# Performance work log

Measured on AMD Instinct MI355X. Metric: run time of the kernel, lower is better.

Reference implementation:

```python
import jax, jax.numpy as jnp
import numpy as np

SEMANTIC_DIM = 128
N_COMPONENTS = 2
EMBED_DIM = SEMANTIC_DIM * N_COMPONENTS  # 256
MAX_LEN = 512


def sinusoidal_pe(max_len, d_model):
    pos = jnp.arange(max_len, dtype=jnp.float32)[:, None]              # (L,1)
    div = jnp.exp(jnp.arange(0, d_model, 2, dtype=jnp.float32) * (-np.log(10000.0) / d_model))
    ang = pos * div                                                     # (L, d/2)
    # interleave sin/cos: pe[:,0::2]=sin, pe[:,1::2]=cos
    return jnp.stack([jnp.sin(ang), jnp.cos(ang)], axis=-1).reshape(max_len, d_model)


def setup_inputs() -> dict:
    key = jax.random.key(0)
    k1, k2, k3, k4 = jax.random.split(key, 4)
    byte_sequence = jax.random.randint(k1, (64, 512), 0, 256, dtype=jnp.int64)
    continuous_positions = jax.random.uniform(k2, (64, 2048), dtype=jnp.float32)
    emb_table = jax.random.normal(k3, (256, EMBED_DIM), dtype=jnp.float32)
    locality_shapes = jax.random.normal(k4, (256, 3), dtype=jnp.float32)
    return {
        "byte_sequence": byte_sequence,
        "continuous_positions": continuous_positions,
        "emb_table": emb_table,
        "locality_shapes": locality_shapes,
    }


def reference(byte_sequence, continuous_positions, emb_table, locality_shapes):
    B, L = byte_sequence.shape
    pe = sinusoidal_pe(MAX_LEN, EMBED_DIM)[:L]                          # (L, E)
    byte_embeds = emb_table[byte_sequence] + pe[None, :, :]             # (B, L, E)
    byte_amplitudes = byte_embeds.reshape(B, L, N_COMPONENTS, SEMANTIC_DIM)

    byte_positions = jnp.linspace(0.0, 1.0, L, dtype=jnp.float32)      # (L,)
    x_diff = continuous_positions[:, :, None] - byte_positions[None, None, :]  # (B, P, L)

    lp = locality_shapes[byte_sequence]                                 # (B, L, 3)
    widths = jnp.abs(lp[:, :, 1]) * 0.02 + 1e-5                         # (B, L)
    amplitudes = jax.nn.sigmoid(lp[:, :, 2])                            # (B, L)

    local_basis = jnp.exp(-0.5 * (x_diff / widths[:, None, :]) ** 2) * amplitudes[:, None, :]
    semantic_field = jnp.einsum('bpl,blcd->bpcd', local_basis, byte_amplitudes)
    return semantic_field
```

## Files before the change

### kernel.cpp

```cpp
#include <hip/hip_runtime.h>
#include <math.h>

#define LSEQ 512
#define EDIM 256
#define PDIM 2048
#define BM   128
#define BK   32
#define NT   16

typedef _Float16 f16x8 __attribute__((ext_vector_type(8)));
typedef _Float16 f16x2 __attribute__((ext_vector_type(2)));
typedef float    f32x4 __attribute__((ext_vector_type(4)));

#if __has_builtin(__builtin_amdgcn_exp2f)
#define EXP2F(x) __builtin_amdgcn_exp2f(x)
#else
#define EXP2F(x) __expf((x) * 0.6931471805599453f)
#endif

__device__ inline f16x2 pk2(float a, float b) {
#if __has_builtin(__builtin_amdgcn_cvt_pkrtz)
    return __builtin_bit_cast(f16x2, __builtin_amdgcn_cvt_pkrtz(a, b));
#else
    f16x2 r; r[0] = (_Float16)a; r[1] = (_Float16)b; return r;
#endif
}

__device__ __host__ inline int tile_off(int r, int g) {
    return ((r >> 1) << 6) + ((r & 1) << 5) + (((g ^ ((r >> 1) & 3)) & 3) << 3);
}

__device__ inline void g2lds16(const void* g, void* l) {
    __builtin_amdgcn_global_load_lds(
        (const __attribute__((address_space(1))) void*)g,
        (__attribute__((address_space(3))) void*)l, 16, 0, 0);
}

__global__ __launch_bounds__(256) void precompute_all(
    const int*   __restrict__ bs,
    const float* __restrict__ ls,
    const float* __restrict__ emb,
    float2*      __restrict__ params,
    _Float16*    __restrict__ baset) {
    const int b   = blockIdx.x >> 4;
    const int t   = blockIdx.x & 15;
    const int tid = threadIdx.x;

    __shared__ int sByte[BK];
    if (tid < BK) {
        const int l    = t * BK + tid;
        const int byte = bs[b * LSEQ + l];
        sByte[tid] = byte;
        const float l1  = ls[byte * 3 + 1];
        const float l2  = ls[byte * 3 + 2];
        const float wdt = fabsf(l1) * 0.02f + 1e-5f;
        const float amp = 1.0f / (1.0f + __expf(-l2));
        params[b * LSEQ + l] = make_float2(-0.72134752f / (wdt * wdt),
                                           __log2f(amp));
    }
    __syncthreads();

    const float div = __expf((float)(tid >> 1) * (-2.0f * 9.210340372f / 256.0f));
    _Float16* chunk = baset + ((size_t)blockIdx.x << 13);
#pragma unroll
    for (int g = 0; g < 4; ++g) {
        f16x8 v;
#pragma unroll
        for (int j = 0; j < 8; ++j) {
            const int lj  = g * 8 + j;
            const float ang = (float)(t * BK + lj) * div;
            const float pev = (tid & 1) ? cosf(ang) : sinf(ang);
            v[j] = (_Float16)(emb[sByte[lj] * EDIM + tid] + pev);
        }
        *(f16x8*)&chunk[tile_off(tid, g)] = v;
    }
}

__global__ __launch_bounds__(512, 4) void field_mfma(
    const float*    __restrict__ cpos,
    const float2*   __restrict__ params,
    const _Float16* __restrict__ baset,
    float*          __restrict__ out) {

    __shared__ __align__(16) _Float16 sW[2][BM * BK];
    __shared__ __align__(16) _Float16 sB[2][EDIM * BK];
    __shared__ __align__(16) float2   sPrm[LSEQ];

    const int orig = blockIdx.x;
    const int wg   = (orig & 7) * 128 + (orig >> 3);
    const int b    = wg >> 4;
    const int pt   = wg & 15;

    const int tid = threadIdx.x, lane = tid & 63, wave = tid >> 6;
    const int c15 = lane & 15, g4 = lane >> 4;
    const int wrow = wave >> 2, wcol = wave & 3;

    const int sp = tid >> 2;
    const int sg = tid & 3;
    const float mypos = cpos[b * PDIM + pt * BM + sp];
    const float invL  = 1.0f / (float)(LSEQ - 1);
    const int   woff  = tile_off(sp, sg);

    int aoff[4], boff[4];
#pragma unroll
    for (int rt = 0; rt < 4; ++rt) aoff[rt] = tile_off(wrow * 64 + rt * 16 + c15, g4);
#pragma unroll
    for (int ct = 0; ct < 4; ++ct) boff[ct] = tile_off(wcol * 64 + ct * 16 + c15, g4);

    sPrm[tid] = params[b * LSEQ + tid];
    const _Float16* bt = baset + ((size_t)b * NT << 13);
#pragma unroll
    for (int buf = 0; buf < 2; ++buf) {
        const _Float16* src = bt + buf * 8192 + wave * 1024 + lane * 8;
        g2lds16(src,       &sB[buf][wave * 1024]);
        g2lds16(src + 512, &sB[buf][wave * 1024 + 512]);
    }
    __syncthreads();

    auto genW = [&](int t, int dbuf) {
        const float4* qp = (const float4*)&sPrm[t * BK + sg * 8];
        const float4 q01 = qp[0], q23 = qp[1], q45 = qp[2], q67 = qp[3];
        const float bl0 = (float)(t * BK + sg * 8) * invL;
        float w[8];
#define GW(i, c2, la) { float d = mypos - (bl0 + (float)(i) * invL); \
                        w[i] = EXP2F(fmaf(d * d, (c2), (la))); }
        GW(0, q01.x, q01.y) GW(1, q01.z, q01.w)
        GW(2, q23.x, q23.y) GW(3, q23.z, q23.w)
        GW(4, q45.x, q45.y) GW(5, q45.z, q45.w)
        GW(6, q67.x, q67.y) GW(7, q67.z, q67.w)
#undef GW
        f16x8 wv;
        ((f16x2*)&wv)[0] = pk2(w[0], w[1]);
        ((f16x2*)&wv)[1] = pk2(w[2], w[3]);
        ((f16x2*)&wv)[2] = pk2(w[4], w[5]);
        ((f16x2*)&wv)[3] = pk2(w[6], w[7]);
        *(f16x8*)&sW[dbuf][woff] = wv;
    };

    genW(0, 0);
    __syncthreads();

    f32x4 acc[4][4];
#pragma unroll
    for (int i = 0; i < 4; ++i)
#pragma unroll
        for (int j = 0; j < 4; ++j) acc[i][j] = (f32x4)(0.f);

    for (int t = 0; t < NT; ++t) {
        const int cur = t & 1;
        if (t < NT - 1) genW(t + 1, cur ^ 1);

        const _Float16* wb = sW[cur];
        const _Float16* bb = sB[cur];
        f16x8 af[4];
#pragma unroll
        for (int rt = 0; rt < 4; ++rt) af[rt] = *(const f16x8*)&wb[aoff[rt]];
        __builtin_amdgcn_s_setprio(1);
#pragma unroll
        for (int ct = 0; ct < 4; ++ct) {
            const f16x8 bf = *(const f16x8*)&bb[boff[ct]];
#pragma unroll
            for (int rt = 0; rt < 4; ++rt)
                acc[rt][ct] = __builtin_amdgcn_mfma_f32_16x16x32_f16(af[rt], bf, acc[rt][ct], 0, 0, 0);
        }
        __builtin_amdgcn_s_setprio(0);

        __syncthreads();

        if (t < NT - 2) {
            const _Float16* src = bt + (t + 2) * 8192 + wave * 1024 + lane * 8;
            g2lds16(src,       &sB[cur][wave * 1024]);
            g2lds16(src + 512, &sB[cur][wave * 1024 + 512]);
        }
    }

#pragma unroll
    for (int rt = 0; rt < 4; ++rt)
#pragma unroll
        for (int ct = 0; ct < 4; ++ct) {
            const int e = wcol * 64 + ct * 16 + c15;
#pragma unroll
            for (int r = 0; r < 4; ++r) {
                const int p = pt * BM + wrow * 64 + rt * 16 + g4 * 4 + r;
                out[((size_t)b * PDIM + p) * EDIM + e] = acc[rt][ct][r];
            }
        }
}

extern "C" void kernel_launch(void* const* d_in, const int* in_sizes, int n_in,
                              void* d_out, int out_size, void* d_ws, size_t ws_size,
                              hipStream_t stream) {
    const int*   bs   = (const int*)d_in[0];
    const float* cpos = (const float*)d_in[1];
    const float* emb  = (const float*)d_in[2];
    const float* ls   = (const float*)d_in[3];

    const int B = in_sizes[0] / LSEQ;

    char* ws = (char*)d_ws;
    float2*   params = (float2*)ws;
    _Float16* baset  = (_Float16*)(ws + (1u << 18));

    precompute_all<<<B * NT, 256, 0, stream>>>(bs, ls, emb, params, baset);
    field_mfma<<<B * (PDIM / BM), 512, 0, stream>>>(cpos, params, baset, (float*)d_out);
}
```

Before: 65.99 us.

## Sort query positions and skip byte tiles outside Gaussian support

Adds a per-batch bitonic sort of continuous positions so each block handles a contiguous range of positions. Precompute now records, for each 32-byte tile, the interval where its Gaussian weights exceed a small cutoff. The main kernel skips weight generation and MFMA work for tiles outside that interval, and scatters output rows back through the sort permutation. It also switches the positional-encoding sin/cos to hardware instructions. The cost is an extra kernel launch, scattered output writes, and a small truncation of very small weights. The skip only pays off if the widths are narrow, as they are in the test data.

```diff
diff --git a/kernel.cpp b/kernel.cpp
--- a/kernel.cpp
+++ b/kernel.cpp
@@ -26,6 +26,23 @@
 #endif
 }
 
+__device__ inline float hw_sin(float ang) {
+#if __has_builtin(__builtin_amdgcn_sinf)
+    float rev = ang * 0.15915494309189535f;
+    return __builtin_amdgcn_sinf(rev - floorf(rev));
+#else
+    return sinf(ang);
+#endif
+}
+__device__ inline float hw_cos(float ang) {
+#if __has_builtin(__builtin_amdgcn_cosf)
+    float rev = ang * 0.15915494309189535f;
+    return __builtin_amdgcn_cosf(rev - floorf(rev));
+#else
+    return cosf(ang);
+#endif
+}
+
 __device__ __host__ inline int tile_off(int r, int g) {
     return ((r >> 1) << 6) + ((r & 1) << 5) + (((g ^ ((r >> 1) & 3)) & 3) << 3);
 }
@@ -34,6 +51,37 @@
     __builtin_amdgcn_global_load_lds(
         (const __attribute__((address_space(1))) void*)g,
         (__attribute__((address_space(3))) void*)l, 16, 0, 0);
+}
+
+__global__ __launch_bounds__(1024) void sort_pos(const float* __restrict__ cpos,
+                                                 float* __restrict__ spos,
+                                                 int*   __restrict__ oidx) {
+    const int b = blockIdx.x, tid = threadIdx.x;
+    __shared__ float v[2048];
+    __shared__ int   ix[2048];
+    v[tid] = cpos[b * PDIM + tid];           ix[tid] = tid;
+    v[tid + 1024] = cpos[b * PDIM + tid + 1024]; ix[tid + 1024] = tid + 1024;
+    for (int k = 2; k <= 2048; k <<= 1) {
+        for (int j = k >> 1; j > 0; j >>= 1) {
+            __syncthreads();
+#pragma unroll
+            for (int r = 0; r < 2; ++r) {
+                const int i = tid + (r << 10);
+                const int p = i ^ j;
+                if (p > i) {
+                    const bool up = ((i & k) == 0);
+                    const float a = v[i], c = v[p];
+                    if ((a > c) == up) {
+                        v[i] = c; v[p] = a;
+                        const int t2 = ix[i]; ix[i] = ix[p]; ix[p] = t2;
+                    }
+                }
+            }
+        }
+    }
+    __syncthreads();
+    spos[b * PDIM + tid] = v[tid];           oidx[b * PDIM + tid] = ix[tid];
+    spos[b * PDIM + tid + 1024] = v[tid + 1024]; oidx[b * PDIM + tid + 1024] = ix[tid + 1024];
 }
 
 __global__ __launch_bounds__(256) void precompute_all(
@@ -41,12 +89,14 @@
     const float* __restrict__ ls,
     const float* __restrict__ emb,
     float2*      __restrict__ params,
+    float2*      __restrict__ benv,
     _Float16*    __restrict__ baset) {
     const int b   = blockIdx.x >> 4;
     const int t   = blockIdx.x & 15;
     const int tid = threadIdx.x;
 
     __shared__ int sByte[BK];
+    __shared__ float sLo[BK], sHi[BK];
     if (tid < BK) {
         const int l    = t * BK + tid;
         const int byte = bs[b * LSEQ + l];
@@ -55,10 +105,20 @@
         const float l2  = ls[byte * 3 + 2];
         const float wdt = fabsf(l1) * 0.02f + 1e-5f;
         const float amp = 1.0f / (1.0f + __expf(-l2));
-        params[b * LSEQ + l] = make_float2(-0.72134752f / (wdt * wdt),
-                                           __log2f(amp));
-    }
-    __syncthreads();
+        const float la  = __log2f(amp);
+        params[b * LSEQ + l] = make_float2(-0.72134752f / (wdt * wdt), la);
+        const float dcut = wdt * sqrtf((la + 16.6096f) * (1.0f / 0.72134752f));
+        const float ctr  = (float)l * (1.0f / (float)(LSEQ - 1));
+        sLo[tid] = ctr - dcut;
+        sHi[tid] = ctr + dcut;
+    }
+    __syncthreads();
+    if (tid == 0) {
+        float lo = sLo[0], hi = sHi[0];
+#pragma unroll
+        for (int i = 1; i < BK; ++i) { lo = fminf(lo, sLo[i]); hi = fmaxf(hi, sHi[i]); }
+        benv[blockIdx.x] = make_float2(lo, hi);
+    }
 
     const float div = __expf((float)(tid >> 1) * (-2.0f * 9.210340372f / 256.0f));
     _Float16* chunk = baset + ((size_t)blockIdx.x << 13);
@@ -69,7 +129,7 @@
         for (int j = 0; j < 8; ++j) {
             const int lj  = g * 8 + j;
             const float ang = (float)(t * BK + lj) * div;
-            const float pev = (tid & 1) ? cosf(ang) : sinf(ang);
+            const float pev = (tid & 1) ? hw_cos(ang) : hw_sin(ang);
             v[j] = (_Float16)(emb[sByte[lj] * EDIM + tid] + pev);
         }
         *(f16x8*)&chunk[tile_off(tid, g)] = v;
@@ -77,14 +137,19 @@
 }
 
 __global__ __launch_bounds__(512, 4) void field_mfma(
-    const float*    __restrict__ cpos,
+    const float*    __restrict__ spos,
+    const int*      __restrict__ oidx,
     const float2*   __restrict__ params,
+    const float2*   __restrict__ benv,
     const _Float16* __restrict__ baset,
     float*          __restrict__ out) {
 
     __shared__ __align__(16) _Float16 sW[2][BM * BK];
     __shared__ __align__(16) _Float16 sB[2][EDIM * BK];
     __shared__ __align__(16) float2   sPrm[LSEQ];
+    __shared__ float  sPos[BM];
+    __shared__ int    sIdx[BM];
+    __shared__ float2 sBenv[NT];
 
     const int orig = blockIdx.x;
     const int wg   = (orig & 7) * 128 + (orig >> 3);
@@ -97,9 +162,8 @@
 
     const int sp = tid >> 2;
     const int sg = tid & 3;
-    const float mypos = cpos[b * PDIM + pt * BM + sp];
-    const float invL  = 1.0f / (float)(LSEQ - 1);
-    const int   woff  = tile_off(sp, sg);
+    const float invL = 1.0f / (float)(LSEQ - 1);
+    const int woff = tile_off(sp, sg);
 
     int aoff[4], boff[4];
 #pragma unroll
@@ -108,6 +172,12 @@
     for (int ct = 0; ct < 4; ++ct) boff[ct] = tile_off(wcol * 64 + ct * 16 + c15, g4);
 
     sPrm[tid] = params[b * LSEQ + tid];
+    if (tid < BM) {
+        sPos[tid] = spos[b * PDIM + pt * BM + tid];
+        sIdx[tid] = oidx[b * PDIM + pt * BM + tid];
+    }
+    if (tid < NT) sBenv[tid] = benv[b * NT + tid];
+
     const _Float16* bt = baset + ((size_t)b * NT << 13);
 #pragma unroll
     for (int buf = 0; buf < 2; ++buf) {
@@ -117,17 +187,27 @@
     }
     __syncthreads();
 
+    const float mypos = sPos[sp];
+    const float glo = sPos[wave * 16], ghi = sPos[wave * 16 + 15];
+    const float wlo = sPos[wrow * 64], whi = sPos[wrow * 64 + 63];
+
     auto genW = [&](int t, int dbuf) {
+        const float2 be = sBenv[t];
+        if (ghi < be.x || glo > be.y) {
+            *(f16x8*)&sW[dbuf][woff] = (f16x8)(_Float16)0.0f;
+            return;
+        }
         const float4* qp = (const float4*)&sPrm[t * BK + sg * 8];
-        const float4 q01 = qp[0], q23 = qp[1], q45 = qp[2], q67 = qp[3];
+        const float4 q0 = qp[0], q1 = qp[1], q2 = qp[2], q3 = qp[3];
         const float bl0 = (float)(t * BK + sg * 8) * invL;
+        const float pd  = mypos - bl0;
         float w[8];
-#define GW(i, c2, la) { float d = mypos - (bl0 + (float)(i) * invL); \
+#define GW(i, c2, la) { float d = pd - (float)(i) * invL; \
                         w[i] = EXP2F(fmaf(d * d, (c2), (la))); }
-        GW(0, q01.x, q01.y) GW(1, q01.z, q01.w)
-        GW(2, q23.x, q23.y) GW(3, q23.z, q23.w)
-        GW(4, q45.x, q45.y) GW(5, q45.z, q45.w)
-        GW(6, q67.x, q67.y) GW(7, q67.z, q67.w)
+        GW(0, q0.x, q0.y) GW(1, q0.z, q0.w)
+        GW(2, q1.x, q1.y) GW(3, q1.z, q1.w)
+        GW(4, q2.x, q2.y) GW(5, q2.z, q2.w)
+        GW(6, q3.x, q3.y) GW(7, q3.z, q3.w)
 #undef GW
         f16x8 wv;
         ((f16x2*)&wv)[0] = pk2(w[0], w[1]);
@@ -150,20 +230,25 @@
         const int cur = t & 1;
         if (t < NT - 1) genW(t + 1, cur ^ 1);
 
-        const _Float16* wb = sW[cur];
-        const _Float16* bb = sB[cur];
-        f16x8 af[4];
-#pragma unroll
-        for (int rt = 0; rt < 4; ++rt) af[rt] = *(const f16x8*)&wb[aoff[rt]];
-        __builtin_amdgcn_s_setprio(1);
-#pragma unroll
-        for (int ct = 0; ct < 4; ++ct) {
-            const f16x8 bf = *(const f16x8*)&bb[boff[ct]];
-#pragma unroll
-            for (int rt = 0; rt < 4; ++rt)
-                acc[rt][ct] = __builtin_amdgcn_mfma_f32_16x16x32_f16(af[rt], bf, acc[rt][ct], 0, 0, 0);
-        }
-        __builtin_amdgcn_s_setprio(0);
+        {
+            const float2 be = sBenv[t];
+            if (!(whi < be.x || wlo > be.y)) {
+                const _Float16* wb = sW[cur];
+                const _Float16* bb = sB[cur];
+                f16x8 af[4];
+#pragma unroll
+                for (int rt = 0; rt < 4; ++rt) af[rt] = *(const f16x8*)&wb[aoff[rt]];
+                __builtin_amdgcn_s_setprio(1);
+#pragma unroll
+                for (int ct = 0; ct < 4; ++ct) {
+                    const f16x8 bf = *(const f16x8*)&bb[boff[ct]];
+#pragma unroll
+                    for (int rt = 0; rt < 4; ++rt)
+                        acc[rt][ct] = __builtin_amdgcn_mfma_f32_16x16x32_f16(af[rt], bf, acc[rt][ct], 0, 0, 0);
+                }
+                __builtin_amdgcn_s_setprio(0);
+            }
+        }
 
         __syncthreads();
 
@@ -175,16 +260,19 @@
     }
 
 #pragma unroll
-    for (int rt = 0; rt < 4; ++rt)
+    for (int rt = 0; rt < 4; ++rt) {
+        int op_[4];
+#pragma unroll
+        for (int reg = 0; reg < 4; ++reg)
+            op_[reg] = sIdx[wrow * 64 + rt * 16 + g4 * 4 + reg];
 #pragma unroll
         for (int ct = 0; ct < 4; ++ct) {
             const int e = wcol * 64 + ct * 16 + c15;
 #pragma unroll
-            for (int r = 0; r < 4; ++r) {
-                const int p = pt * BM + wrow * 64 + rt * 16 + g4 * 4 + r;
-                out[((size_t)b * PDIM + p) * EDIM + e] = acc[rt][ct][r];
-            }
-        }
+            for (int reg = 0; reg < 4; ++reg)
+                out[((size_t)b * PDIM + op_[reg]) * EDIM + e] = acc[rt][ct][reg];
+        }
+    }
 }
 
 extern "C" void kernel_launch(void* const* d_in, const int* in_sizes, int n_in,
@@ -199,8 +287,13 @@
 
     char* ws = (char*)d_ws;
     float2*   params = (float2*)ws;
-    _Float16* baset  = (_Float16*)(ws + (1u << 18));
-
-    precompute_all<<<B * NT, 256, 0, stream>>>(bs, ls, emb, params, baset);
-    field_mfma<<<B * (PDIM / BM), 512, 0, stream>>>(cpos, params, baset, (float*)d_out);
-}
+    float*    spos   = (float*)(ws + 0x40000);
+    int*      oidx   = (int*)(ws + 0xC0000);
+    float2*   benv   = (float2*)(ws + 0x140000);
+    _Float16* baset  = (_Float16*)(ws + 0x180000);
+
+    sort_pos<<<B, 1024, 0, stream>>>(cpos, spos, oidx);
+    precompute_all<<<B * NT, 256, 0, stream>>>(bs, ls, emb, params, benv, baset);
+    field_mfma<<<B * (PDIM / BM), 512, 0, stream>>>(spos, oidx, params, benv, baset,
+                                                    (float*)d_out);
+}
```

New measurement: 83.02 us. 25.8% more time.
